# Kernel optimization log

Hardware: AMD Instinct MI355X
Metric: run time of the kernel (lower is better)

The kernel has to match this reference:

```python
import jax, jax.numpy as jnp
import numpy as np

D_MODEL = 1024
H = 16
D_K = D_MODEL // H
NEG = -10000.0


def setup_inputs() -> dict:
    key = jax.random.key(0)
    ks = jax.random.split(key, 8)
    B, L = 2, 2048
    q = jax.random.normal(ks[0], (B, L, D_MODEL), dtype=jnp.float32)
    k = jax.random.normal(ks[1], (B, L, D_MODEL), dtype=jnp.float32)
    v = jax.random.normal(ks[2], (B, L, D_MODEL), dtype=jnp.float32)
    mask = jax.random.randint(ks[3], (B, 1, 1, L), 0, 2, dtype=jnp.int32)
    s = 1.0 / np.sqrt(D_MODEL)
    w_q = jax.random.normal(ks[4], (D_MODEL, D_MODEL), dtype=jnp.float32) * s
    w_k = jax.random.normal(ks[5], (D_MODEL, D_MODEL), dtype=jnp.float32) * s
    w_v = jax.random.normal(ks[6], (D_MODEL, D_MODEL), dtype=jnp.float32) * s
    w_o = jax.random.normal(ks[7], (D_MODEL, D_MODEL), dtype=jnp.float32) * s
    return {"q": q, "k": k, "v": v, "mask": mask,
            "w_q": w_q, "w_k": w_k, "w_v": w_v, "w_o": w_o}


def reference(q, k, v, mask, w_q, w_k, w_v, w_o):
    B, Lq, _ = q.shape
    Lk = k.shape[1]
    # projections; nn.Linear applies x @ W.T
    qh = (q @ w_q.T).reshape(B, Lq, H, D_K).transpose(0, 2, 1, 3)  # [B,H,Lq,Dk]
    kh = (k @ w_k.T).reshape(B, Lk, H, D_K).transpose(0, 2, 1, 3)
    vh = (v @ w_v.T).reshape(B, Lk, H, D_K).transpose(0, 2, 1, 3)
    scale = 1.0 / jnp.sqrt(jnp.asarray(D_K, dtype=qh.dtype))
    scores = jnp.einsum("bhqd,bhkd->bhqk", qh, kh) * scale  # [B,H,Lq,Lk]
    scores = jnp.where(mask == 0, jnp.asarray(NEG, scores.dtype), scores)
    attn = jax.nn.softmax(scores, axis=-1)
    out = jnp.einsum("bhqk,bhkd->bhqd", attn, vh)  # [B,H,Lq,Dk]
    out = out.transpose(0, 2, 1, 3).reshape(B, Lq, D_MODEL)
    return out @ w_o.T
```

## Files before the change

### kernel.cpp

```cpp
#include <hip/hip_runtime.h>
#include <hip/hip_bf16.h>


using bf8   = __attribute__((ext_vector_type(8))) short;
using f4    = __attribute__((ext_vector_type(4))) float;
using f16v  = __attribute__((ext_vector_type(16))) float;
using u32x4 = __attribute__((ext_vector_type(4))) unsigned int;

__device__ __forceinline__ short f2bf(float f) {
  unsigned u = __float_as_uint(f);
  u = (u + 0x7FFFu + ((u >> 16) & 1u)) >> 16;
  return (short)(unsigned short)u;
}

__device__ __forceinline__ unsigned cvt_pk_bf16(float lo, float hi) {
  unsigned r;
  asm("v_cvt_pk_bf16_f32 %0, %1, %2" : "=v"(r) : "v"(lo), "v"(hi));
  return r;
}

__device__ __forceinline__ void permswap(unsigned &a, unsigned &b) {
  asm volatile("v_permlane32_swap_b32 %0, %1" : "+v"(a), "+v"(b));
}

__global__ __launch_bounds__(256)
void cast_bf16(const float* __restrict__ q, const float* __restrict__ k,
               const float* __restrict__ v, const float* __restrict__ wq,
               const float* __restrict__ wk, const float* __restrict__ wv,
               const float* __restrict__ wo,
               short* __restrict__ qc, short* __restrict__ kc, short* __restrict__ vc,
               short* __restrict__ wqc, short* __restrict__ wkc, short* __restrict__ wvc,
               short* __restrict__ woc)
{
  const int z = blockIdx.z;
  if (z >= 3 && blockIdx.x >= 512) return;
  const float* src = (z==0)?q:(z==1)?k:(z==2)?v:(z==3)?wq:(z==4)?wk:(z==5)?wv:wo;
  short* dst       = (z==0)?qc:(z==1)?kc:(z==2)?vc:(z==3)?wqc:(z==4)?wkc:(z==5)?wvc:woc;
  long i = ((long)blockIdx.x * 256 + threadIdx.x) * 8;
  const float4* s4 = (const float4*)(src + i);
  float4 a = s4[0], b = s4[1];
  u32x4 pk;
  pk[0] = cvt_pk_bf16(a.x, a.y);
  pk[1] = cvt_pk_bf16(a.z, a.w);
  pk[2] = cvt_pk_bf16(b.x, b.y);
  pk[3] = cvt_pk_bf16(b.z, b.w);
  *(bf8*)(dst + i) = __builtin_bit_cast(bf8, pk);
}

template<bool HEADOUT>
__device__ __forceinline__ void gemm_body(const short* __restrict__ Ain,
                                          const short* __restrict__ W,
                                          void* __restrict__ Out,
                                          int bm, int bn, float scale)
{
  constexpr int LDT = 40;
  __shared__ short As[2][128 * LDT];
  __shared__ short Ws[2][128 * LDT];

  const int tid  = threadIdx.x;
  const int lane = tid & 63;
  const int wv   = tid >> 6;
  const int wm = wv >> 1, wn = wv & 1;
  const int l15 = lane & 15;
  const int lk8 = (lane >> 4) * 8;

  const f4 fz = {0.f, 0.f, 0.f, 0.f};
  f4 acc[4][4];
  #pragma unroll
  for (int mi = 0; mi < 4; ++mi)
    #pragma unroll
    for (int ni = 0; ni < 4; ++ni) acc[mi][ni] = fz;

  const int arow = tid >> 1;
  const int acol = (tid & 1) * 16;

  bf8 ar[2], wr[2];

  auto loadA = [&](int kt) {
    const short* src = Ain + (long)(bm + arow) * 1024 + kt + acol;
    ar[0] = *(const bf8*)src;
    ar[1] = *(const bf8*)(src + 8);
  };
  auto loadW = [&](int kt) {
    const short* src = W + (long)(bn + arow) * 1024 + kt + acol;
    wr[0] = *(const bf8*)src;
    wr[1] = *(const bf8*)(src + 8);
  };
  auto writeTile = [&](int buf) {
    short* ap = &As[buf][arow * LDT + acol];
    *(bf8*)ap     = ar[0];
    *(bf8*)(ap+8) = ar[1];
    short* wp = &Ws[buf][arow * LDT + acol];
    *(bf8*)wp     = wr[0];
    *(bf8*)(wp+8) = wr[1];
  };

  loadA(0); loadW(0); writeTile(0);
  __syncthreads();

  for (int ktI = 0; ktI < 32; ++ktI) {
    const int cur = ktI & 1;
    if (ktI < 31) { loadA((ktI + 1) * 32); loadW((ktI + 1) * 32); }

    bf8 af[4], bfr[4];
    #pragma unroll
    for (int mi = 0; mi < 4; ++mi)
      af[mi] = *(const bf8*)&As[cur][(wm*64 + mi*16 + l15) * LDT + lk8];
    #pragma unroll
    for (int ni = 0; ni < 4; ++ni)
      bfr[ni] = *(const bf8*)&Ws[cur][(wn*64 + ni*16 + l15) * LDT + lk8];
    #pragma unroll
    for (int mi = 0; mi < 4; ++mi)
      #pragma unroll
      for (int ni = 0; ni < 4; ++ni)
        acc[mi][ni] = __builtin_amdgcn_mfma_f32_16x16x32_bf16(af[mi], bfr[ni], acc[mi][ni], 0, 0, 0);

    if (ktI < 31) writeTile(cur ^ 1);
    __syncthreads();
  }

  #pragma unroll
  for (int mi = 0; mi < 4; ++mi) {
    #pragma unroll
    for (int ni = 0; ni < 4; ++ni) {
      #pragma unroll
      for (int r = 0; r < 4; ++r) {
        int mg = bm + wm*64 + mi*16 + (lane >> 4)*4 + r;
        int ng = bn + wn*64 + ni*16 + l15;
        float val = acc[mi][ni][r] * scale;
        if constexpr (HEADOUT) {
          int b = mg >> 11, l = mg & 2047;
          int h = ng >> 6,  d = ng & 63;
          ((short*)Out)[(((long)(b*16 + h) * 2048 + l) << 6) + d] = f2bf(val);
        } else {
          ((float*)Out)[(long)mg * 1024 + ng] = val;
        }
      }
    }
  }
}

__global__ __launch_bounds__(256)
void qkv_gemm(const short* __restrict__ qc, const short* __restrict__ kc,
              const short* __restrict__ vc, const short* __restrict__ wqc,
              const short* __restrict__ wkc, const short* __restrict__ wvc,
              short* __restrict__ qh, short* __restrict__ kh, short* __restrict__ vh)
{
  const int z = blockIdx.z;
  const short* A = (z == 0) ? qc : (z == 1) ? kc : vc;
  const short* W = (z == 0) ? wqc : (z == 1) ? wkc : wvc;
  short* Out     = (z == 0) ? qh : (z == 1) ? kh : vh;
  const float scale = (z == 0) ? 0.18033688f : 1.0f;
  gemm_body<true>(A, W, Out, blockIdx.x * 128, blockIdx.y * 128, scale);
}

__global__ __launch_bounds__(256)
void out_gemm(const short* __restrict__ att, const short* __restrict__ woc,
              float* __restrict__ out)
{
  gemm_body<false>(att, woc, out, blockIdx.x * 128, blockIdx.y * 128, 1.0f);
}

__global__ __launch_bounds__(512, 2)
void attn_fwd(const short* __restrict__ qh, const short* __restrict__ kh,
              const short* __restrict__ vh, const int* __restrict__ mask,
              short* __restrict__ att)
{
  __shared__ short Kb[2][128 * 64];
  __shared__ short Vb[2][64 * 128];
  __shared__ short biasB[2][128];

  const int t = threadIdx.x, lane = t & 63, w = t >> 6;
  const int l31 = lane & 31, hi = lane >> 5;
  const unsigned swz = (unsigned)((l31 & 7) << 4);
  const int bh = blockIdx.x, b = bh >> 4, h = bh & 15;
  const int qrow0 = blockIdx.y * 256 + w * 32;
  const long base = (long)bh * 2048 * 64;

  bf8 qb[4];
  {
    const short* qp = qh + base + (long)(qrow0 + l31) * 64 + hi * 8;
    #pragma unroll
    for (int s = 0; s < 4; ++s) qb[s] = *(const bf8*)(qp + s * 16);
  }
  bf8 qb4;
  #pragma unroll
  for (int i = 0; i < 8; ++i) qb4[i] = 0;
  qb4[0] = hi ? (short)0 : (short)0x3F80;
  bf8 ones;
  #pragma unroll
  for (int i = 0; i < 8; ++i) ones[i] = (l31 == 0) ? (short)0x3F80 : (short)0;

  f16v o0, o1, o2, fz16;
  #pragma unroll
  for (int i = 0; i < 16; ++i) { o0[i] = 0.f; o1[i] = 0.f; o2[i] = 0.f; fz16[i] = 0.f; }

  const int sr = t & 63, c8 = (t >> 6) << 3;
  const short* kgp = kh + base + c8;
  const short* vgp = vh + base + c8;
  const unsigned kwb = (unsigned)(sr * 128 + c8 * 2) ^ ((unsigned)(sr & 7) << 4);

  {
    bf8 kr  = *(const bf8*)(kgp + (long)sr * 64);
    bf8 kr2 = *(const bf8*)(kgp + (long)(64 + sr) * 64);
    bf8 vr  = *(const bf8*)(vgp + (long)sr * 64);
    bf8 vr2 = *(const bf8*)(vgp + (long)(64 + sr) * 64);
    *(bf8*)((char*)Kb[0] + kwb)        = kr;
    *(bf8*)((char*)Kb[0] + kwb + 8192) = kr2;
    #pragma unroll
    for (int i = 0; i < 8; ++i) {
      unsigned a0 = (unsigned)((c8 + i) * 256 + sr * 2)        ^ ((unsigned)(i & 7) << 4);
      unsigned a1 = (unsigned)((c8 + i) * 256 + (64 + sr) * 2) ^ ((unsigned)(i & 7) << 4);
      *(short*)((char*)Vb[0] + a0) = vr[i];
      *(short*)((char*)Vb[0] + a1) = vr2[i];
    }
    if (t < 128) biasB[0][t] = mask[b * 2048 + t] ? (short)0xC139 : (short)0xC680;
  }
  __syncthreads();

  for (int it = 0; it < 16; ++it) {
    const int cur = it & 1;
    bf8 kr, kr2, vr, vr2; int mv = 1;
    if (it < 15) {
      const int kt = (it + 1) * 128;
      kr  = *(const bf8*)(kgp + (long)(kt + sr) * 64);
      kr2 = *(const bf8*)(kgp + (long)(kt + 64 + sr) * 64);
      vr  = *(const bf8*)(vgp + (long)(kt + sr) * 64);
      vr2 = *(const bf8*)(vgp + (long)(kt + 64 + sr) * 64);
      if (t < 128) mv = mask[b * 2048 + kt + t];
    }

    const char* Kc = (const char*)Kb[cur];
    const char* Vc = (const char*)Vb[cur];

    #pragma unroll
    for (int ha = 0; ha < 2; ++ha) {
      const int ko = ha * 64;

      f16v sT[2];
      #pragma unroll
      for (int kb2 = 0; kb2 < 2; ++kb2) {
        bf8 ba;
        #pragma unroll
        for (int i = 0; i < 8; ++i) ba[i] = 0;
        ba[0] = hi ? (short)0 : biasB[cur][ko + kb2 * 32 + l31];
        sT[kb2] = __builtin_amdgcn_mfma_f32_32x32x16_bf16(ba, qb4, fz16, 0, 0, 0);
        #pragma unroll
        for (int s = 0; s < 4; ++s) {
          unsigned ab = (unsigned)((ko + kb2 * 32 + l31) * 128 + s * 32 + hi * 16) ^ swz;
          bf8 ka = *(const bf8*)(Kc + ab);
          sT[kb2] = __builtin_amdgcn_mfma_f32_32x32x16_bf16(ka, qb[s], sT[kb2], 0, 0, 0);
        }
      }

      unsigned Lh[16], Hh[16];
      #pragma unroll
      for (int t2 = 0; t2 < 2; ++t2)
        #pragma unroll
        for (int pi = 0; pi < 8; ++pi) {
          float pe0 = exp2f(sT[t2][2*pi]);
          float pe1 = exp2f(sT[t2][2*pi+1]);
          unsigned pkv = cvt_pk_bf16(pe0, pe1);
          unsigned Lv = pkv, Hv = pkv;
          permswap(Lv, Hv);
          Lh[t2*8 + pi] = Lv; Hh[t2*8 + pi] = Hv;
        }

      #pragma unroll
      for (int t2 = 0; t2 < 2; ++t2)
        #pragma unroll
        for (int sl = 0; sl < 2; ++sl) {
          const int bx = t2*8 + sl*4;
          u32x4 tmp;
          tmp[0] = hi ? Lh[bx+2] : Lh[bx+0];
          tmp[1] = hi ? Lh[bx+3] : Lh[bx+1];
          tmp[2] = hi ? Hh[bx+2] : Hh[bx+0];
          tmp[3] = hi ? Hh[bx+3] : Hh[bx+1];
          bf8 pa = __builtin_bit_cast(bf8, tmp);
          const int sg = t2*2 + sl;
          bf8 v0f = *(const bf8*)(Vc + ((unsigned)((0*32 + l31)*256 + ko*2 + sg*32 + hi*16) ^ swz));
          o0 = __builtin_amdgcn_mfma_f32_32x32x16_bf16(pa, v0f, o0, 0, 0, 0);
          bf8 v1f = *(const bf8*)(Vc + ((unsigned)((1*32 + l31)*256 + ko*2 + sg*32 + hi*16) ^ swz));
          o1 = __builtin_amdgcn_mfma_f32_32x32x16_bf16(pa, v1f, o1, 0, 0, 0);
          o2 = __builtin_amdgcn_mfma_f32_32x32x16_bf16(pa, ones, o2, 0, 0, 0);
        }
    }

    if (it < 15) {
      const int nxt = cur ^ 1;
      *(bf8*)((char*)Kb[nxt] + kwb)        = kr;
      *(bf8*)((char*)Kb[nxt] + kwb + 8192) = kr2;
      #pragma unroll
      for (int i = 0; i < 8; ++i) {
        unsigned a0 = (unsigned)((c8 + i) * 256 + sr * 2)        ^ ((unsigned)(i & 7) << 4);
        unsigned a1 = (unsigned)((c8 + i) * 256 + (64 + sr) * 2) ^ ((unsigned)(i & 7) << 4);
        *(short*)((char*)Vb[nxt] + a0) = vr[i];
        *(short*)((char*)Vb[nxt] + a1) = vr2[i];
      }
      if (t < 128) biasB[nxt][t] = mv ? (short)0xC139 : (short)0xC680;
    }
    __syncthreads();
  }

  #pragma unroll
  for (int r = 0; r < 16; ++r) {
    int qr = (r & 3) + 8 * (r >> 2) + 4 * hi;
    float ls = __shfl(o2[r], hi << 5);
    float inv = 1.0f / ls;
    long rowb = (long)(b * 2048 + qrow0 + qr) * 1024 + h * 64;
    att[rowb + l31]      = f2bf(o0[r] * inv);
    att[rowb + 32 + l31] = f2bf(o1[r] * inv);
  }
}

extern "C" void kernel_launch(void* const* d_in, const int* in_sizes, int n_in,
                              void* d_out, int out_size, void* d_ws, size_t ws_size,
                              hipStream_t stream) {
  const float* q    = (const float*)d_in[0];
  const float* k    = (const float*)d_in[1];
  const float* v    = (const float*)d_in[2];
  const int*   mask = (const int*)d_in[3];
  const float* w_q  = (const float*)d_in[4];
  const float* w_k  = (const float*)d_in[5];
  const float* w_v  = (const float*)d_in[6];
  const float* w_o  = (const float*)d_in[7];
  float* out = (float*)d_out;

  char* ws = (char*)d_ws;
  const long HSZ = 2L * 16 * 2048 * 64 * sizeof(short);
  const long WSZ = 1024L * 1024 * sizeof(short);
  short* qh  = (short*)(ws);
  short* kh  = (short*)(ws + HSZ);
  short* vh  = (short*)(ws + 2 * HSZ);
  short* att = (short*)(ws + 3 * HSZ);
  short* qc  = (short*)(ws + 4 * HSZ);
  short* kc  = (short*)(ws + 5 * HSZ);
  short* vc  = (short*)(ws + 6 * HSZ);
  short* wqc = (short*)(ws + 7 * HSZ);
  short* wkc = (short*)(ws + 7 * HSZ + WSZ);
  short* wvc = (short*)(ws + 7 * HSZ + 2 * WSZ);
  short* woc = (short*)(ws + 7 * HSZ + 3 * WSZ);

  cast_bf16<<<dim3(2048, 1, 7), 256, 0, stream>>>(q, k, v, w_q, w_k, w_v, w_o,
                                                  qc, kc, vc, wqc, wkc, wvc, woc);
  qkv_gemm<<<dim3(32, 8, 3), 256, 0, stream>>>(qc, kc, vc, wqc, wkc, wvc, qh, kh, vh);
  attn_fwd<<<dim3(32, 8), dim3(512), 0, stream>>>(qh, kh, vh, mask, att);
  out_gemm<<<dim3(32, 8), 256, 0, stream>>>(att, woc, out);
}
```

Measured before the change: 139.6 us.

## Split attention over key range into two partial blocks with combine kernel

Measured after the change: 152.0 us. +8.9%, slower.

```diff
diff --git a/kernel.cpp b/kernel.cpp
--- a/kernel.cpp
+++ b/kernel.cpp
@@ -161,10 +161,11 @@
   gemm_body<false>(att, woc, out, blockIdx.x * 128, blockIdx.y * 128, 1.0f);
 }
 
+template<bool SPLIT>
 __global__ __launch_bounds__(512, 2)
 void attn_fwd(const short* __restrict__ qh, const short* __restrict__ kh,
               const short* __restrict__ vh, const int* __restrict__ mask,
-              short* __restrict__ att)
+              short* __restrict__ att, float* __restrict__ PO, float* __restrict__ PL)
 {
   __shared__ short Kb[2][128 * 64];
   __shared__ short Vb[2][64 * 128];
@@ -175,6 +176,9 @@
   const unsigned swz = (unsigned)((l31 & 7) << 4);
   const int bh = blockIdx.x, b = bh >> 4, h = bh & 15;
   const int qrow0 = blockIdx.y * 256 + w * 32;
+  const int z = SPLIT ? blockIdx.z : 0;
+  const int kbase = z * 1024;
+  const int NITER = SPLIT ? 8 : 16;
   const long base = (long)bh * 2048 * 64;
 
   bf8 qb[4];
@@ -196,8 +200,8 @@
   for (int i = 0; i < 16; ++i) { o0[i] = 0.f; o1[i] = 0.f; o2[i] = 0.f; fz16[i] = 0.f; }
 
   const int sr = t & 63, c8 = (t >> 6) << 3;
-  const short* kgp = kh + base + c8;
-  const short* vgp = vh + base + c8;
+  const short* kgp = kh + base + (long)kbase * 64 + c8;
+  const short* vgp = vh + base + (long)kbase * 64 + c8;
   const unsigned kwb = (unsigned)(sr * 128 + c8 * 2) ^ ((unsigned)(sr & 7) << 4);
 
   {
@@ -214,20 +218,20 @@
       *(short*)((char*)Vb[0] + a0) = vr[i];
       *(short*)((char*)Vb[0] + a1) = vr2[i];
     }
-    if (t < 128) biasB[0][t] = mask[b * 2048 + t] ? (short)0xC139 : (short)0xC680;
+    if (t < 128) biasB[0][t] = mask[b * 2048 + kbase + t] ? (short)0xC139 : (short)0xC680;
   }
   __syncthreads();
 
-  for (int it = 0; it < 16; ++it) {
+  for (int it = 0; it < NITER; ++it) {
     const int cur = it & 1;
     bf8 kr, kr2, vr, vr2; int mv = 1;
-    if (it < 15) {
+    if (it < NITER - 1) {
       const int kt = (it + 1) * 128;
       kr  = *(const bf8*)(kgp + (long)(kt + sr) * 64);
       kr2 = *(const bf8*)(kgp + (long)(kt + 64 + sr) * 64);
       vr  = *(const bf8*)(vgp + (long)(kt + sr) * 64);
       vr2 = *(const bf8*)(vgp + (long)(kt + 64 + sr) * 64);
-      if (t < 128) mv = mask[b * 2048 + kt + t];
+      if (t < 128) mv = mask[b * 2048 + kbase + kt + t];
     }
 
     const char* Kc = (const char*)Kb[cur];
@@ -286,7 +290,7 @@
         }
     }
 
-    if (it < 15) {
+    if (it < NITER - 1) {
       const int nxt = cur ^ 1;
       *(bf8*)((char*)Kb[nxt] + kwb)        = kr;
       *(bf8*)((char*)Kb[nxt] + kwb + 8192) = kr2;
@@ -302,15 +306,54 @@
     __syncthreads();
   }
 
-  #pragma unroll
-  for (int r = 0; r < 16; ++r) {
-    int qr = (r & 3) + 8 * (r >> 2) + 4 * hi;
-    float ls = __shfl(o2[r], hi << 5);
-    float inv = 1.0f / ls;
-    long rowb = (long)(b * 2048 + qrow0 + qr) * 1024 + h * 64;
-    att[rowb + l31]      = f2bf(o0[r] * inv);
-    att[rowb + 32 + l31] = f2bf(o1[r] * inv);
-  }
+  if constexpr (SPLIT) {
+    const long prow = ((long)(z * 32 + bh)) * 2048 + qrow0;
+    #pragma unroll
+    for (int r = 0; r < 16; ++r) {
+      int qr = (r & 3) + 8 * (r >> 2) + 4 * hi;
+      PO[(prow + qr) * 64 + l31]      = o0[r];
+      PO[(prow + qr) * 64 + 32 + l31] = o1[r];
+      if (l31 == 0) PL[prow + qr] = o2[r];
+    }
+  } else {
+    #pragma unroll
+    for (int r = 0; r < 16; ++r) {
+      int qr = (r & 3) + 8 * (r >> 2) + 4 * hi;
+      float ls = __shfl(o2[r], hi << 5);
+      float inv = 1.0f / ls;
+      long rowb = (long)(b * 2048 + qrow0 + qr) * 1024 + h * 64;
+      att[rowb + l31]      = f2bf(o0[r] * inv);
+      att[rowb + 32 + l31] = f2bf(o1[r] * inv);
+    }
+  }
+}
+
+__global__ __launch_bounds__(256)
+void combine_attn(const float* __restrict__ PO, const float* __restrict__ PL,
+                  short* __restrict__ att)
+{
+  const int gid = blockIdx.x * 256 + threadIdx.x;
+  const int rowid = gid >> 3;
+  const int bh = rowid >> 11, l = rowid & 2047;
+  const int d0 = (gid & 7) * 8;
+  const long zs = 32L * 2048 * 64;
+  const long pb = (long)rowid * 64 + d0;
+  float4 a0 = *(const float4*)(PO + pb);
+  float4 a1 = *(const float4*)(PO + pb + 4);
+  float4 b0 = *(const float4*)(PO + zs + pb);
+  float4 b1 = *(const float4*)(PO + zs + pb + 4);
+  float inv = 1.0f / (PL[rowid] + PL[32L * 2048 + rowid]);
+  const int b = bh >> 4, h = bh & 15;
+  bf8 o;
+  o[0] = f2bf((a0.x + b0.x) * inv);
+  o[1] = f2bf((a0.y + b0.y) * inv);
+  o[2] = f2bf((a0.z + b0.z) * inv);
+  o[3] = f2bf((a0.w + b0.w) * inv);
+  o[4] = f2bf((a1.x + b1.x) * inv);
+  o[5] = f2bf((a1.y + b1.y) * inv);
+  o[6] = f2bf((a1.z + b1.z) * inv);
+  o[7] = f2bf((a1.w + b1.w) * inv);
+  *(bf8*)(att + (long)(b * 2048 + l) * 1024 + h * 64 + d0) = o;
 }
 
 extern "C" void kernel_launch(void* const* d_in, const int* in_sizes, int n_in,
@@ -333,17 +376,29 @@
   short* kh  = (short*)(ws + HSZ);
   short* vh  = (short*)(ws + 2 * HSZ);
   short* att = (short*)(ws + 3 * HSZ);
-  short* qc  = (short*)(ws + 4 * HSZ);
-  short* kc  = (short*)(ws + 5 * HSZ);
-  short* vc  = (short*)(ws + 6 * HSZ);
-  short* wqc = (short*)(ws + 7 * HSZ);
-  short* wkc = (short*)(ws + 7 * HSZ + WSZ);
-  short* wvc = (short*)(ws + 7 * HSZ + 2 * WSZ);
-  short* woc = (short*)(ws + 7 * HSZ + 3 * WSZ);
+  short* woc = (short*)(ws + 4 * HSZ);
+  char*  C0  = ws + 4 * HSZ + WSZ;
+  short* qc  = (short*)(C0);
+  short* kc  = (short*)(C0 + HSZ);
+  short* vc  = (short*)(C0 + 2 * HSZ);
+  short* wqc = (short*)(C0 + 3 * HSZ);
+  short* wkc = (short*)(C0 + 3 * HSZ + WSZ);
+  short* wvc = (short*)(C0 + 3 * HSZ + 2 * WSZ);
+  float* PO  = (float*)(C0);
+  float* PL  = (float*)(C0 + 2L * 32 * 2048 * 64 * sizeof(float));
+  const size_t needed = (size_t)(4 * HSZ + WSZ)
+                      + 2L * 32 * 2048 * 64 * sizeof(float)
+                      + 2L * 32 * 2048 * sizeof(float);
+  const bool split = ws_size >= needed;
 
   cast_bf16<<<dim3(2048, 1, 7), 256, 0, stream>>>(q, k, v, w_q, w_k, w_v, w_o,
                                                   qc, kc, vc, wqc, wkc, wvc, woc);
   qkv_gemm<<<dim3(32, 8, 3), 256, 0, stream>>>(qc, kc, vc, wqc, wkc, wvc, qh, kh, vh);
-  attn_fwd<<<dim3(32, 8), dim3(512), 0, stream>>>(qh, kh, vh, mask, att);
+  if (split) {
+    attn_fwd<true><<<dim3(32, 8, 2), dim3(512), 0, stream>>>(qh, kh, vh, mask, att, PO, PL);
+    combine_attn<<<2048, 256, 0, stream>>>(PO, PL, att);
+  } else {
+    attn_fwd<false><<<dim3(32, 8), dim3(512), 0, stream>>>(qh, kh, vh, mask, att, PO, PL);
+  }
   out_gemm<<<dim3(32, 8), 256, 0, stream>>>(att, woc, out);
 }
```
